# Performance work log

Hardware: AMD Instinct MI355X
Metric: run time of the kernel (lower is better)

The kernel has to match this reference:

```python
import jax, jax.numpy as jnp
import numpy as np

B, L, N, FA, FB, D, OUT, R, T = 128, 128, 6, 39, 10, 200, 1, 3, 2
MB = 256  # num bonds per molecule
NEG = -9e8


def setup_inputs():
    key = jax.random.key(0)
    ks = iter(jax.random.split(key, 64))
    def rn(shape, sc=0.05):
        return jax.random.normal(next(ks), shape, dtype=jnp.float32) * sc
    inp = {}
    inp['atom_list'] = jax.random.normal(next(ks), (B, L, FA), dtype=jnp.float32)
    inp['bond_list'] = jax.random.normal(next(ks), (B, MB, FB), dtype=jnp.float32)
    inp['atom_degree_list'] = jax.random.randint(next(ks), (B, L, N), 0, L, dtype=jnp.int32)
    inp['bond_degree_list'] = jax.random.randint(next(ks), (B, L, N), 0, MB, dtype=jnp.int32)
    inp['atom_mask'] = jnp.ones((B, L), dtype=jnp.float32)
    # parameters (torch Linear: y = x @ W + b with W stored here as [in, out])
    inp['W_atom'] = rn((FA, D)); inp['b_atom'] = rn((D,))
    inp['W_nei'] = rn((FA + FB, D)); inp['b_nei'] = rn((D,))
    inp['W_align'] = rn((R, 2 * D, 1)); inp['b_align'] = rn((R, 1))
    inp['W_attend'] = rn((R, D, D)); inp['b_attend'] = rn((R, D))
    # GRUCell weights, torch layout [3D, D], gate order r,z,n
    inp['Wih'] = rn((R, 3 * D, D)); inp['Whh'] = rn((R, 3 * D, D))
    inp['bih'] = rn((R, 3 * D)); inp['bhh'] = rn((R, 3 * D))
    inp['W_mol_align'] = rn((2 * D, 1)); inp['b_mol_align'] = rn((1,))
    inp['W_mol_attend'] = rn((D, D)); inp['b_mol_attend'] = rn((D,))
    inp['mWih'] = rn((3 * D, D)); inp['mWhh'] = rn((3 * D, D))
    inp['mbih'] = rn((3 * D,)); inp['mbhh'] = rn((3 * D,))
    inp['W_metric'] = rn((2 * D, D)); inp['b_metric'] = rn((D,))
    inp['W_out'] = rn((D, OUT)); inp['b_out'] = rn((OUT,))
    return inp


def _gather(feat, idx):
    # feat [B, M, F], idx [B, L, N] -> [B, L, N, F]
    b, l, n = idx.shape
    g = jnp.take_along_axis(feat, idx.reshape(b, l * n)[..., None], axis=1)
    return g.reshape(b, l, n, feat.shape[-1])


def _gru(x, h, Wih, Whh, bih, bhh):
    gi = x @ Wih.T + bih
    gh = h @ Whh.T + bhh
    ir, iz, inn = jnp.split(gi, 3, axis=-1)
    hr, hz, hn = jnp.split(gh, 3, axis=-1)
    r = jax.nn.sigmoid(ir + hr)
    z = jax.nn.sigmoid(iz + hz)
    n = jnp.tanh(inn + r * hn)
    return (1.0 - z) * n + z * h


def reference(atom_list, bond_list, atom_degree_list, bond_degree_list, atom_mask,
              W_atom, b_atom, W_nei, b_nei, W_align, b_align, W_attend, b_attend,
              Wih, Whh, bih, bhh, W_mol_align, b_mol_align, W_mol_attend, b_mol_attend,
              mWih, mWhh, mbih, mbhh, W_metric, b_metric, W_out, b_out):
    lrelu = jax.nn.leaky_relu
    b, l, _ = atom_list.shape
    atom_feature = lrelu(atom_list @ W_atom + b_atom)          # [B,L,D]
    atom_nei = _gather(atom_list, atom_degree_list)            # [B,L,N,FA]
    bond_nei = _gather(bond_list, bond_degree_list)            # [B,L,N,FB]
    nei = lrelu(jnp.concatenate([atom_nei, bond_nei], -1) @ W_nei + b_nei)  # [B,L,N,D]

    pad = (atom_degree_list == l - 1)
    attend_mask = (~pad).astype(jnp.float32)[..., None]        # [B,L,N,1]
    softmax_mask = jnp.where(pad, NEG, 0.0)[..., None]         # [B,L,N,1]

    h = atom_feature
    cur = atom_feature
    for r in range(R):
        if r > 0:
            nei = _gather(cur, atom_degree_list)
        exp = jnp.broadcast_to(cur[:, :, None, :], nei.shape)
        align = lrelu(jnp.concatenate([exp, nei], -1) @ W_align[r] + b_align[r])
        w = jax.nn.softmax(align + softmax_mask, axis=-2) * attend_mask
        trans = nei @ W_attend[r] + b_attend[r]
        ctx = jax.nn.elu(jnp.sum(w * trans, axis=-2))          # [B,L,D]
        h = _gru(ctx.reshape(-1, D), h.reshape(-1, D), Wih[r], Whh[r], bih[r], bhh[r]).reshape(b, l, D)
        cur = jax.nn.relu(h)

    am = atom_mask[..., None]                                   # [B,L,1]
    mol_feature = jnp.sum(cur * am, axis=-2)                    # [B,D]
    act_mol = jax.nn.relu(mol_feature)
    mol_softmax_mask = jnp.where(am == 0.0, NEG, 0.0)           # [B,L,1]
    for _ in range(T):
        exp = jnp.broadcast_to(act_mol[:, None, :], cur.shape)
        score = lrelu(jnp.concatenate([exp, cur], -1) @ W_mol_align + b_mol_align)
        w = jax.nn.softmax(score + mol_softmax_mask, axis=-2) * am
        trans = cur @ W_mol_attend + b_mol_attend
        ctx = jax.nn.elu(jnp.sum(w * trans, axis=-2))           # [B,D]
        mol_feature = _gru(ctx, mol_feature, mWih, mWhh, mbih, mbhh)
        act_mol = jax.nn.relu(mol_feature)

    dd = jnp.float32(R - 2)  # leaked python loop var `d` in the original
    feat = jnp.concatenate([mol_feature, mol_feature + dd], -1)
    return (feat @ W_metric + b_metric) @ W_out + b_out


if __name__ == '__main__':
    out = reference(**setup_inputs())
    print(out.shape)
```

## Files before the change

### kernel.cpp

```cpp
#include <hip/hip_runtime.h>
#include <hip/hip_bf16.h>
#include <math.h>
#include <string.h>

#define B_ 128
#define L_ 128
#define N_ 6
#define FA_ 39
#define FB_ 10
#define D_ 200
#define MB_ 256
#define R_ 3
#define T_ 2
#define NEGV -9e8f
#define BL_ (B_*L_)
#define G3D_ (3*D_)
#define FP32TAG 0x3F800000u
#define KP 416
#define NP 896
#define KC 224
#define NC 256

typedef __hip_bfloat16 bf16;
typedef __attribute__((ext_vector_type(8))) short short8;
typedef __attribute__((ext_vector_type(4))) float f32x4;

__device__ __forceinline__ float b2f(const bf16 x){ return __bfloat162float(x); }
__device__ __forceinline__ unsigned short f2b(float v){ bf16 t = __float2bfloat16(v); return *reinterpret_cast<unsigned short*>(&t); }
__device__ __forceinline__ float bu2f(unsigned short u){ unsigned x = ((unsigned)u)<<16; float f; memcpy(&f,&x,4); return f; }
__device__ __forceinline__ float lreluf(float x){ return x>=0.f ? x : 0.01f*x; }
__device__ __forceinline__ float eluf(float x){ return x>0.f ? x : expm1f(x); }
__device__ __forceinline__ float sigmf(float x){ return 1.f/(1.f+expf(-x)); }

#define NSEG 14
struct CvtArgs { const void* src[NSEG]; int ofs[NSEG+1]; };

#define PREPB_N (R_*NP*KP)
#define PREPW_N (R_*NC*KC)
#define PREPM_N (D_*G3D_)
#define PREPT_N 40000
#define PREPE_N 80000
#define CONV_N 23989
#define XHPAD_N (BL_*16)
#define AROWS (BL_ + B_*MB_)
#define A_N (AROWS*64)
#define BI_N (448*64)

struct PrepArgs {
    CvtArgs cvt;
    const void *Wih, *Whh, *Watt, *mWih, *mWhh, *Wmt, *Wme;
    const void *bond, *Wnei, *atom, *Watom;
    float* conv;
    unsigned short *B2t, *WatT, *mTi, *mTh, *Wmt16, *Wme16, *XH, *A16, *Bi16;
    const unsigned* amtag;
    int ew_total;
};

__device__ __forceinline__ float ldd(const void* p, size_t i, bool f32){
    return f32 ? ((const float*)p)[i] : b2f(((const bf16*)p)[i]);
}

__global__ void __launch_bounds__(256) k_prep(PrepArgs A){
    bool f32 = (*A.amtag == FP32TAG);
    int i = blockIdx.x*256 + (int)threadIdx.x;
    if (i >= A.ew_total) return;
    if (i < CONV_N){
        int s = 0;
        while (i >= A.cvt.ofs[s+1]) s++;
        A.conv[i] = ldd(A.cvt.src[s], i - A.cvt.ofs[s], f32);
        return;
    }
    int i2 = i - CONV_N;
    if (i2 < PREPB_N){
        int kk = i2 % KP;
        int rest = i2 / KP;
        int n = rest % NP;
        int r = rest / NP;
        float v = 0.f;
        if (kk < 200){
            if (n < 600) v = ldd(A.Wih, ((size_t)(r*G3D_ + n))*D_ + kk, f32);
        } else if (kk < 400){
            int j = -1;
            if (n < 400) j = n;
            else if (n >= 600 && n < 800) j = n - 200;
            if (j >= 0) v = ldd(A.Whh, ((size_t)(r*G3D_ + j))*D_ + (kk-200), f32);
        }
        A.B2t[i2] = f2b(v);
        return;
    }
    int i3 = i2 - PREPB_N;
    if (i3 < PREPW_N){
        int kk = i3 % KC;
        int rest = i3 / KC;
        int n = rest % NC;
        int r = rest / NC;
        float v = 0.f;
        if (kk < 200 && n < 200) v = ldd(A.Watt, ((size_t)r*D_ + kk)*D_ + n, f32);
        A.WatT[i3] = f2b(v);
        return;
    }
    int i4 = i3 - PREPW_N;
    if (i4 < PREPM_N){
        int j = i4 % G3D_, k = i4 / G3D_;
        size_t si = (size_t)j*D_ + k;
        A.mTi[i4] = f2b(ldd(A.mWih, si, f32));
        A.mTh[i4] = f2b(ldd(A.mWhh, si, f32));
        return;
    }
    int i5 = i4 - PREPM_N;
    if (i5 < PREPT_N){
        A.Wmt16[i5] = f2b(ldd(A.Wmt, i5, f32));
        return;
    }
    int i6 = i5 - PREPT_N;
    if (i6 < PREPE_N){
        A.Wme16[i6] = f2b(ldd(A.Wme, i6, f32));
        return;
    }
    int i7 = i6 - PREPE_N;
    if (i7 < XHPAD_N){
        int al = i7 >> 4, j = i7 & 15;
        A.XH[(size_t)al*KP + 400 + j] = 0;
        return;
    }
    int i8 = i7 - XHPAD_N;
    if (i8 < A_N){
        int row = i8 >> 6, k = i8 & 63;
        float v = 0.f;
        if (row < BL_){
            if (k < FA_) v = ldd(A.atom, (size_t)row*FA_ + k, f32);
        } else {
            int rb = row - BL_;
            if (k >= FA_ && k < FA_+FB_) v = ldd(A.bond, (size_t)rb*FB_ + (k-FA_), f32);
        }
        A.A16[i8] = f2b(v);
        return;
    }
    int i9 = i8 - A_N;
    if (i9 < BI_N){
        int n = i9 >> 6, k = i9 & 63;
        float v = 0.f;
        if (n < 200){
            if (k < FA_) v = ldd(A.Watom, (size_t)k*D_ + n, f32);
        } else if (n < 400){
            if (k < FA_+FB_) v = ldd(A.Wnei, (size_t)k*D_ + (n-200), f32);
        }
        A.Bi16[i9] = f2b(v);
    }
}

__global__ void __launch_bounds__(256) k_initmm(const unsigned short* __restrict__ A16,
        const unsigned short* __restrict__ Bi16,
        const void* __restrict__ batom, const void* __restrict__ bnei,
        unsigned short* __restrict__ XH, unsigned short* __restrict__ P16,
        unsigned short* __restrict__ Q16, const unsigned* __restrict__ amtag){
    __shared__ unsigned short As[128][40];
    __shared__ unsigned short Bs[64][40];
    bool f32 = (*amtag == FP32TAG);
    int tid = threadIdx.x;
    int mt = (int)blockIdx.x / 7, nt = (int)blockIdx.x % 7;
    int m0 = mt*128, n0 = nt*64;
    if (m0 >= BL_ && n0 + 64 <= 200) return;
    int lane = tid & 63, wv = tid >> 6;
    int quad = lane >> 4, lm = lane & 15;
    f32x4 acc[2][4];
    #pragma unroll
    for (int a=0;a<2;a++)
        #pragma unroll
        for (int b=0;b<4;b++) acc[a][b] = (f32x4){0.f,0.f,0.f,0.f};
    for (int ks = 0; ks < 2; ks++){
        int r0_ = tid >> 2, c0 = (tid & 3) * 8;
        int r1_ = (tid + 256) >> 2, c1 = ((tid + 256) & 3) * 8;
        uint4 a0 = *(const uint4*)&A16[(size_t)(m0 + r0_)*64 + ks*32 + c0];
        uint4 a1 = *(const uint4*)&A16[(size_t)(m0 + r1_)*64 + ks*32 + c1];
        uint4 b0 = *(const uint4*)&Bi16[(size_t)(n0 + (tid >> 2))*64 + ks*32 + (tid & 3)*8];
        __syncthreads();
        *(uint4*)&As[r0_][c0] = a0;
        *(uint4*)&As[r1_][c1] = a1;
        *(uint4*)&Bs[tid >> 2][(tid & 3)*8] = b0;
        __syncthreads();
        short8 av0 = *(const short8*)&As[wv*32 + lm][quad*8];
        short8 av1 = *(const short8*)&As[wv*32 + 16 + lm][quad*8];
        #pragma unroll
        for (int ns=0; ns<4; ns++){
            short8 bv = *(const short8*)&Bs[ns*16 + lm][quad*8];
            acc[0][ns] = __builtin_amdgcn_mfma_f32_16x16x32_bf16(av0, bv, acc[0][ns], 0,0,0);
            acc[1][ns] = __builtin_amdgcn_mfma_f32_16x16x32_bf16(av1, bv, acc[1][ns], 0,0,0);
        }
    }
    #pragma unroll
    for (int ms=0; ms<2; ms++)
      #pragma unroll
      for (int ns=0; ns<4; ns++){
        int n = n0 + ns*16 + lm;
        #pragma unroll
        for (int i=0;i<4;i++){
            int row = m0 + wv*32 + ms*16 + quad*4 + i;
            float v = acc[ms][ns][i];
            if (row < BL_){
                if (n < 200){
                    XH[(size_t)row*KP + 200 + n] = f2b(lreluf(v + ldd(batom, n, f32)));
                } else if (n < 400){
                    P16[(size_t)row*D_ + (n-200)] = f2b(v + ldd(bnei, n-200, f32));
                }
            } else if (n >= 200 && n < 400){
                Q16[(size_t)(row-BL_)*D_ + (n-200)] = f2b(v);
            }
        }
      }
}

__global__ void __launch_bounds__(256) k_attn(
        const unsigned short* __restrict__ cur16, const unsigned short* __restrict__ XH,
        const float* __restrict__ s1, const float* __restrict__ tb,
        const int* __restrict__ adl, const int* __restrict__ bdl,
        const unsigned short* __restrict__ P16, const unsigned short* __restrict__ Q16,
        const float* __restrict__ W_align, const float* __restrict__ b_align, int r,
        unsigned short* __restrict__ wnei, float* __restrict__ wsum){
    int bid = blockIdx.x;
    int mol = bid & (B_-1), chunk = bid >> 7;
    int wv = threadIdx.x >> 6, lane = threadIdx.x & 63;
    int al = mol*L_ + chunk*4 + wv;
    __shared__ float s_nei[4][N_][D_];

    int idxn[N_]; bool pad[N_];
    for (int n=0;n<N_;n++){ idxn[n] = adl[al*N_ + n]; pad[n] = (idxn[n] == L_-1); }

    float s2[N_];
    float s1v;
    if (r == 0){
        for (int j = lane; j < N_*D_; j += 64){
            int n = j / D_, d = j - n*D_;
            int bd = bdl[al*N_ + n];
            float acc = bu2f(P16[((size_t)mol*L_ + idxn[n])*D_ + d])
                      + bu2f(Q16[((size_t)mol*MB_ + bd)*D_ + d]);
            s_nei[wv][n][d] = lreluf(acc);
        }
        const float* Wab = W_align + D_;
        for (int n=0;n<N_;n++){
            float acc = 0.f;
            for (int d=lane; d<D_; d+=64) acc += s_nei[wv][n][d] * Wab[d];
            for (int o=32;o>0;o>>=1) acc += __shfl_xor(acc,o);
            s2[n] = acc;
        }
        float a1 = 0.f;
        for (int d=lane; d<D_; d+=64) a1 += bu2f(XH[(size_t)al*KP + 200 + d]) * W_align[d];
        for (int o=32;o>0;o>>=1) a1 += __shfl_xor(a1,o);
        s1v = a1;
    } else {
        float tmp = 0.f;
        if (lane < N_) tmp = tb[mol*L_ + idxn[lane]];
        for (int n=0;n<N_;n++) s2[n] = __shfl(tmp, n);
        s1v = s1[al];
    }

    float bav = b_align[r];
    float a[N_]; float mx = -1e30f;
    for (int n=0;n<N_;n++){
        float v = lreluf(s1v + s2[n] + bav);
        if (pad[n]) v += NEGV;
        a[n] = v; mx = fmaxf(mx, v);
    }
    float w[N_]; float se = 0.f;
    for (int n=0;n<N_;n++){ float e = expf(a[n]-mx); w[n]=e; se += e; }
    float inv = 1.f/se; float wsv = 0.f;
    for (int n=0;n<N_;n++){ w[n] = pad[n] ? 0.f : w[n]*inv; wsv += w[n]; }

    if (r == 0){
        for (int d=lane; d<D_; d+=64){
            float acc = 0.f;
            #pragma unroll
            for (int n=0;n<N_;n++) acc += w[n] * s_nei[wv][n][d];
            wnei[(size_t)al*KC + d] = f2b(acc);
        }
    } else {
        for (int d=lane; d<D_; d+=64){
            float acc = 0.f;
            #pragma unroll
            for (int n=0;n<N_;n++) acc += w[n] * bu2f(cur16[((size_t)mol*L_ + idxn[n])*KC + d]);
            wnei[(size_t)al*KC + d] = f2b(acc);
        }
    }
    if (lane < 24) wnei[(size_t)al*KC + 200 + lane] = 0;
    if (lane==0) wsum[al] = wsv;
}

__global__ void __launch_bounds__(256) k_ctxmfma(const unsigned short* __restrict__ Wn,
        const float* __restrict__ wsum, const unsigned short* __restrict__ WatT,
        const float* __restrict__ bias, int r, unsigned short* __restrict__ XH){
    __shared__ unsigned short As[128][40];
    __shared__ unsigned short Bs[64][40];
    int tid = threadIdx.x;
    int m0 = ((int)blockIdx.x & 127) * 128;
    int n0 = ((int)blockIdx.x >> 7) * 64;
    const unsigned short* Bt = WatT + (size_t)r*NC*KC;
    int lane = tid & 63, wv = tid >> 6;
    int quad = lane >> 4, lm = lane & 15;
    f32x4 acc[2][4];
    #pragma unroll
    for (int a=0;a<2;a++)
        #pragma unroll
        for (int b=0;b<4;b++) acc[a][b] = (f32x4){0.f,0.f,0.f,0.f};
    for (int ks = 0; ks < 7; ks++){
        int r0_ = tid >> 2, c0 = (tid & 3) * 8;
        int r1_ = (tid + 256) >> 2, c1 = ((tid + 256) & 3) * 8;
        uint4 a0 = *(const uint4*)&Wn[(size_t)(m0 + r0_)*KC + ks*32 + c0];
        uint4 a1 = *(const uint4*)&Wn[(size_t)(m0 + r1_)*KC + ks*32 + c1];
        uint4 b0 = *(const uint4*)&Bt[(size_t)(n0 + (tid >> 2))*KC + ks*32 + (tid & 3)*8];
        __syncthreads();
        *(uint4*)&As[r0_][c0] = a0;
        *(uint4*)&As[r1_][c1] = a1;
        *(uint4*)&Bs[tid >> 2][(tid & 3)*8] = b0;
        __syncthreads();
        short8 av0 = *(const short8*)&As[wv*32 + lm][quad*8];
        short8 av1 = *(const short8*)&As[wv*32 + 16 + lm][quad*8];
        #pragma unroll
        for (int ns=0; ns<4; ns++){
            short8 bv = *(const short8*)&Bs[ns*16 + lm][quad*8];
            acc[0][ns] = __builtin_amdgcn_mfma_f32_16x16x32_bf16(av0, bv, acc[0][ns], 0,0,0);
            acc[1][ns] = __builtin_amdgcn_mfma_f32_16x16x32_bf16(av1, bv, acc[1][ns], 0,0,0);
        }
    }
    #pragma unroll
    for (int ms=0; ms<2; ms++)
      #pragma unroll
      for (int ns=0; ns<4; ns++){
        int n = n0 + ns*16 + lm;
        if (n < 200){
            float bv = bias[r*D_ + n];
            #pragma unroll
            for (int i=0;i<4;i++){
                int row = m0 + wv*32 + ms*16 + quad*4 + i;
                float v = acc[ms][ns][i] + wsum[row]*bv;
                XH[(size_t)row*KP + n] = f2b(eluf(v));
            }
        }
      }
}

__global__ void __launch_bounds__(256) k_gemm(const unsigned short* __restrict__ XH,
        const unsigned short* __restrict__ B2t, unsigned short* __restrict__ C, int r){
    __shared__ unsigned short As[128][40];
    __shared__ unsigned short Bs[128][40];
    int tid = threadIdx.x;
    int m0 = ((int)blockIdx.x & 127) * 128;
    int n0 = ((int)blockIdx.x >> 7) * 128;
    const unsigned short* Bt = B2t + (size_t)r*NP*KP;
    int lane = tid & 63, wv = tid >> 6;
    int quad = lane >> 4, lm = lane & 15;
    f32x4 acc[2][8];
    #pragma unroll
    for (int a=0;a<2;a++)
        #pragma unroll
        for (int b=0;b<8;b++) acc[a][b] = (f32x4){0.f,0.f,0.f,0.f};
    for (int ks = 0; ks < 13; ks++){
        int r0_ = tid >> 2, c0 = (tid & 3) * 8;
        int r1_ = (tid + 256) >> 2, c1 = ((tid + 256) & 3) * 8;
        uint4 a0 = *(const uint4*)&XH[(size_t)(m0 + r0_)*KP + ks*32 + c0];
        uint4 a1 = *(const uint4*)&XH[(size_t)(m0 + r1_)*KP + ks*32 + c1];
        uint4 b0 = *(const uint4*)&Bt[(size_t)(n0 + r0_)*KP + ks*32 + c0];
        uint4 b1 = *(const uint4*)&Bt[(size_t)(n0 + r1_)*KP + ks*32 + c1];
        __syncthreads();
        *(uint4*)&As[r0_][c0] = a0;
        *(uint4*)&As[r1_][c1] = a1;
        *(uint4*)&Bs[r0_][c0] = b0;
        *(uint4*)&Bs[r1_][c1] = b1;
        __syncthreads();
        short8 av0 = *(const short8*)&As[wv*32 + lm][quad*8];
        short8 av1 = *(const short8*)&As[wv*32 + 16 + lm][quad*8];
        #pragma unroll
        for (int ns=0; ns<8; ns++){
            short8 bv = *(const short8*)&Bs[ns*16 + lm][quad*8];
            acc[0][ns] = __builtin_amdgcn_mfma_f32_16x16x32_bf16(av0, bv, acc[0][ns], 0,0,0);
            acc[1][ns] = __builtin_amdgcn_mfma_f32_16x16x32_bf16(av1, bv, acc[1][ns], 0,0,0);
        }
    }
    #pragma unroll
    for (int ms=0; ms<2; ms++)
      #pragma unroll
      for (int ns=0; ns<8; ns++)
        #pragma unroll
        for (int i=0;i<4;i++){
            int row = m0 + wv*32 + ms*16 + quad*4 + i;
            C[(size_t)row*NP + n0 + ns*16 + lm] = f2b(acc[ms][ns][i]);
        }
}

__global__ void __launch_bounds__(256) k_gru2(const unsigned short* __restrict__ C,
        unsigned short* __restrict__ XH, unsigned short* __restrict__ cur16,
        const float* __restrict__ bih, const float* __restrict__ bhh,
        const float* __restrict__ W_align, const float* __restrict__ Wma, int r,
        float* __restrict__ s1, float* __restrict__ tb, float* __restrict__ curdot){
    int wv = threadIdx.x >> 6, lane = threadIdx.x & 63;
    int al = blockIdx.x*4 + wv;
    size_t base = (size_t)al*NP;
    const float* bi = bih + r*G3D_;
    const float* bh = bhh + r*G3D_;
    const float* Wa = W_align + (r+1)*2*D_;
    bool last = (r == R_-1);
    float a1 = 0.f, a2 = 0.f;
    for (int j = lane; j < D_; j += 64){
        float rsum = bu2f(C[base + j]);
        float zsum = bu2f(C[base + 200 + j]);
        float gin  = bu2f(C[base + 400 + j]);
        float ghn  = bu2f(C[base + 600 + j]);
        float rr = sigmf(rsum + bi[j] + bh[j]);
        float zz = sigmf(zsum + bi[D_+j] + bh[D_+j]);
        float nn = tanhf(gin + bi[2*D_+j] + rr*(ghn + bh[2*D_+j]));
        size_t hx = (size_t)al*KP + 200 + j;
        float hv = bu2f(XH[hx]);
        float hn = (1.f-zz)*nn + zz*hv;
        XH[hx] = f2b(hn);
        float cv = fmaxf(hn, 0.f);
        cur16[(size_t)al*KC + j] = f2b(cv);
        if (last){
            a1 += cv * Wma[D_+j];
        } else {
            a1 += cv * Wa[j];
            a2 += cv * Wa[D_+j];
        }
    }
    if (lane < 24) cur16[(size_t)al*KC + 200 + lane] = 0;
    for (int o=32;o>0;o>>=1){ a1 += __shfl_xor(a1,o); a2 += __shfl_xor(a2,o); }
    if (lane==0){
        if (last) curdot[al] = a1;
        else { s1[al] = a1; tb[al] = a2; }
    }
}

__device__ __forceinline__ float brSum(float v, float* s_red){
    for (int o=32;o>0;o>>=1) v += __shfl_xor(v,o);
    int lane = threadIdx.x & 63, wid = threadIdx.x >> 6;
    __syncthreads();
    if (lane==0) s_red[wid] = v;
    __syncthreads();
    float r = 0.f;
    int nw = blockDim.x >> 6;
    for (int i=0;i<nw;i++) r += s_red[i];
    return r;
}

__device__ __forceinline__ float brMax(float v, float* s_red){
    for (int o=32;o>0;o>>=1) v = fmaxf(v, __shfl_xor(v,o));
    int lane = threadIdx.x & 63, wid = threadIdx.x >> 6;
    __syncthreads();
    if (lane==0) s_red[wid] = v;
    __syncthreads();
    float r = s_red[0];
    int nw = blockDim.x >> 6;
    for (int i=1;i<nw;i++) r = fmaxf(r, s_red[i]);
    return r;
}

__global__ void __launch_bounds__(512) k_mol(const unsigned short* __restrict__ cur16,
    const float* __restrict__ curdot, const float* __restrict__ atom_mask,
    const float* __restrict__ Wma, const float* __restrict__ bma,
    const unsigned short* __restrict__ Wmt16, const float* __restrict__ bmt,
    const unsigned short* __restrict__ mTi, const unsigned short* __restrict__ mTh,
    const float* __restrict__ mbih, const float* __restrict__ mbhh,
    const unsigned short* __restrict__ Wme16, const float* __restrict__ bme,
    const float* __restrict__ Wout, const float* __restrict__ bout,
    void* __restrict__ out, const unsigned* __restrict__ amtag){
    int b = blockIdx.x, tid = threadIdx.x;
    int dq = tid & 255, cq = tid >> 8;
    __shared__ unsigned short s_cur[L_*KC];
    __shared__ float s_am[L_], s_neg[L_], s_cd[L_], s_w[L_];
    __shared__ float s_mf[D_], s_act[D_], s_wc[D_], s_ctx[D_];
    __shared__ float s_gi[G3D_], s_gh[G3D_];
    __shared__ float s_part[2][256];
    __shared__ float s_red[8];
    const uint4* src = (const uint4*)(cur16 + (size_t)b*L_*KC);
    for (int i = tid; i < L_*KC/8; i += 512) ((uint4*)s_cur)[i] = src[i];
    if (tid < L_){
        float am = atom_mask[b*L_ + tid];
        s_am[tid] = am;
        s_neg[tid] = (am == 0.f) ? NEGV : 0.f;
        s_cd[tid] = curdot[b*L_ + tid];
    }
    __syncthreads();
    {
        float a0 = 0.f, a1 = 0.f;
        if (dq < D_)
            for (int l=cq*64; l<cq*64+64; l+=2){
                a0 += bu2f(s_cur[l*KC + dq]) * s_am[l];
                a1 += bu2f(s_cur[(l+1)*KC + dq]) * s_am[l+1];
            }
        s_part[cq][dq] = a0 + a1;
        __syncthreads();
        if (tid < D_){
            float v = s_part[0][tid] + s_part[1][tid];
            s_mf[tid] = v; s_act[tid] = fmaxf(v, 0.f);
        }
        __syncthreads();
    }
    float bma0 = bma[0];
    for (int t=0;t<T_;t++){
        float p = (tid < D_) ? s_act[tid] * Wma[tid] : 0.f;
        float s1v = brSum(p, s_red);
        float sc = (tid < L_) ? (lreluf(s1v + s_cd[tid] + bma0) + s_neg[tid]) : -1e30f;
        float mx = brMax(sc, s_red);
        float e = (tid < L_) ? expf(sc - mx) : 0.f;
        float se = brSum(e, s_red);
        float wv_ = (tid < L_) ? e/se*s_am[tid] : 0.f;
        if (tid < L_) s_w[tid] = wv_;
        float wsm = brSum(wv_, s_red);
        __syncthreads();
        {
            float a0 = 0.f, a1 = 0.f;
            if (dq < D_)
                for (int l=cq*64; l<cq*64+64; l+=2){
                    a0 += s_w[l] * bu2f(s_cur[l*KC + dq]);
                    a1 += s_w[l+1] * bu2f(s_cur[(l+1)*KC + dq]);
                }
            s_part[cq][dq] = a0 + a1;
            __syncthreads();
            if (tid < D_) s_wc[tid] = s_part[0][tid] + s_part[1][tid];
            __syncthreads();
        }
        {
            float a0 = 0.f, a1 = 0.f;
            if (dq < D_)
                for (int k=cq*100; k<cq*100+100; k+=2){
                    a0 += s_wc[k] * bu2f(Wmt16[(size_t)k*D_ + dq]);
                    a1 += s_wc[k+1] * bu2f(Wmt16[(size_t)(k+1)*D_ + dq]);
                }
            s_part[cq][dq] = a0 + a1;
            __syncthreads();
            if (tid < D_)
                s_ctx[tid] = eluf(s_part[0][tid] + s_part[1][tid] + wsm * bmt[tid]);
            __syncthreads();
        }
        for (int j=tid; j<G3D_; j+=512){
            float ai0=0.f, ai1=0.f, ai2=0.f, ai3=0.f;
            float ah0=0.f, ah1=0.f, ah2=0.f, ah3=0.f;
            for (int k=0;k<D_;k+=4){
                ai0 += s_ctx[k]   * bu2f(mTi[(size_t)k*G3D_ + j]);
                ai1 += s_ctx[k+1] * bu2f(mTi[(size_t)(k+1)*G3D_ + j]);
                ai2 += s_ctx[k+2] * bu2f(mTi[(size_t)(k+2)*G3D_ + j]);
                ai3 += s_ctx[k+3] * bu2f(mTi[(size_t)(k+3)*G3D_ + j]);
                ah0 += s_mf[k]    * bu2f(mTh[(size_t)k*G3D_ + j]);
                ah1 += s_mf[k+1]  * bu2f(mTh[(size_t)(k+1)*G3D_ + j]);
                ah2 += s_mf[k+2]  * bu2f(mTh[(size_t)(k+2)*G3D_ + j]);
                ah3 += s_mf[k+3]  * bu2f(mTh[(size_t)(k+3)*G3D_ + j]);
            }
            s_gi[j] = (ai0+ai1)+(ai2+ai3); s_gh[j] = (ah0+ah1)+(ah2+ah3);
        }
        __syncthreads();
        if (tid < D_){
            int d = tid;
            float rr = sigmf(s_gi[d] + mbih[d] + s_gh[d] + mbhh[d]);
            float zz = sigmf(s_gi[D_+d] + mbih[D_+d] + s_gh[D_+d] + mbhh[D_+d]);
            float nn = tanhf(s_gi[2*D_+d] + mbih[2*D_+d] + rr*(s_gh[2*D_+d] + mbhh[2*D_+d]));
            float nm = (1.f-zz)*nn + zz*s_mf[d];
            s_mf[d] = nm; s_act[d] = fmaxf(nm, 0.f);
        }
        __syncthreads();
    }
    const float dd = (float)(R_ - 2);
    {
        float a0 = 0.f, a1 = 0.f;
        if (dq < D_)
            for (int k=cq*100; k<cq*100+100; k+=2){
                float mf0 = s_mf[k], mf1 = s_mf[k+1];
                a0 += mf0 * bu2f(Wme16[(size_t)k*D_ + dq])
                    + (mf0 + dd) * bu2f(Wme16[(size_t)(D_+k)*D_ + dq]);
                a1 += mf1 * bu2f(Wme16[(size_t)(k+1)*D_ + dq])
                    + (mf1 + dd) * bu2f(Wme16[(size_t)(D_+k+1)*D_ + dq]);
            }
        s_part[cq][dq] = a0 + a1;
        __syncthreads();
        float p = 0.f;
        if (tid < D_)
            p = (s_part[0][tid] + s_part[1][tid] + bme[tid]) * Wout[tid];
        float o = brSum(p, s_red);
        if (tid==0){
            o += bout[0];
            if (*amtag == FP32TAG) ((float*)out)[b] = o;
            else ((bf16*)out)[b] = __float2bfloat16(o);
        }
    }
}

extern "C" void kernel_launch(void* const* d_in, const int* in_sizes, int n_in,
                              void* d_out, int out_size, void* d_ws, size_t ws_size,
                              hipStream_t stream) {
    const int* adl = (const int*)d_in[2];
    const int* bdl = (const int*)d_in[3];
    const unsigned* amtag = (const unsigned*)d_in[4];

    static const int srcidx[NSEG] = {4,9,10,12,15,16,17,18,20,23,24,26,27,28};
    static const int segsz[NSEG]  = {16384,1200,3,600,1800,1800,400,1,200,600,600,200,200,1};
    CvtArgs ca;
    int ofs[NSEG+1]; ofs[0] = 0;
    for (int i=0;i<NSEG;i++){ ca.src[i] = d_in[srcidx[i]]; ca.ofs[i] = ofs[i]; ofs[i+1] = ofs[i] + segsz[i]; }
    ca.ofs[NSEG] = ofs[NSEG];

    float* ws   = (float*)d_ws;
    float* conv = ws;
    unsigned short* XH    = (unsigned short*)(conv + 24000);
    unsigned short* B2t   = XH + (size_t)BL_*KP;
    unsigned short* WatT  = B2t + PREPB_N;
    unsigned short* mTi   = WatT + PREPW_N;
    unsigned short* mTh   = mTi + PREPM_N;
    unsigned short* Wmt16 = mTh + PREPM_N;
    unsigned short* Wme16 = Wmt16 + PREPT_N;
    unsigned short* Bi16  = Wme16 + PREPE_N;
    unsigned short* cur16 = Bi16 + BI_N;
    unsigned short* creg  = cur16 + (size_t)BL_*KC;
    unsigned short* C = creg;
    unsigned short* A16  = creg;
    unsigned short* wnei = creg;
    unsigned short* Q16  = creg + (size_t)BL_*KC;
    unsigned short* P16  = Q16 + (size_t)B_*MB_*D_;
    float* s1     = (float*)(creg + (size_t)BL_*NP);
    float* tb     = s1 + BL_;
    float* wsum   = tb + BL_;
    float* curdot = wsum + BL_;

    const float* c_amask = conv + ofs[0];
    const float* c_Walign= conv + ofs[1];
    const float* c_balign= conv + ofs[2];
    const float* c_batt  = conv + ofs[3];
    const float* c_bih   = conv + ofs[4];
    const float* c_bhh   = conv + ofs[5];
    const float* c_Wma   = conv + ofs[6];
    const float* c_bma   = conv + ofs[7];
    const float* c_bmt   = conv + ofs[8];
    const float* c_mbih  = conv + ofs[9];
    const float* c_mbhh  = conv + ofs[10];
    const float* c_bme   = conv + ofs[11];
    const float* c_Wout  = conv + ofs[12];
    const float* c_bout  = conv + ofs[13];

    PrepArgs A;
    A.cvt = ca;
    A.Wih = d_in[13]; A.Whh = d_in[14]; A.Watt = d_in[11];
    A.mWih = d_in[21]; A.mWhh = d_in[22]; A.Wmt = d_in[19]; A.Wme = d_in[25];
    A.bond = d_in[1]; A.Wnei = d_in[7]; A.atom = d_in[0]; A.Watom = d_in[5];
    A.conv = conv;
    A.B2t = B2t; A.WatT = WatT; A.mTi = mTi; A.mTh = mTh;
    A.Wmt16 = Wmt16; A.Wme16 = Wme16; A.XH = XH; A.A16 = A16; A.Bi16 = Bi16;
    A.amtag = amtag;
    A.ew_total = CONV_N + PREPB_N + PREPW_N + PREPM_N + PREPT_N + PREPE_N
               + XHPAD_N + A_N + BI_N;

    k_prep<<<(A.ew_total + 255)/256, 256, 0, stream>>>(A);
    k_initmm<<<(AROWS/128)*7, 256, 0, stream>>>(A16, Bi16, d_in[6], d_in[8],
                                                XH, P16, Q16, amtag);

    for (int r=0; r<R_; r++){
        k_attn<<<BL_/4, 256, 0, stream>>>(cur16, XH, s1, tb, adl, bdl, P16, Q16,
                                          c_Walign, c_balign, r, wnei, wsum);
        k_ctxmfma<<<(BL_/128)*(NC/64), 256, 0, stream>>>(wnei, wsum, WatT, c_batt, r, XH);
        k_gemm<<<(BL_/128)*(NP/128), 256, 0, stream>>>(XH, B2t, C, r);
        k_gru2<<<BL_/4, 256, 0, stream>>>(C, XH, cur16, c_bih, c_bhh,
                                          c_Walign, c_Wma, r, s1, tb, curdot);
    }

    k_mol<<<B_, 512, 0, stream>>>(cur16, curdot, c_amask, c_Wma, c_bma, Wmt16, c_bmt,
                                  mTi, mTh, c_mbih, c_mbhh, Wme16, c_bme, c_Wout, c_bout,
                                  d_out, amtag);
}
```

Baseline: 454.5 us.

## Fuse GRU gate epilogue into gate GEMM with interleaved weights and ping-pong hidden buffers

```diff
diff --git a/kernel.cpp b/kernel.cpp
--- a/kernel.cpp
+++ b/kernel.cpp
@@ -41,7 +41,9 @@
 #define PREPT_N 40000
 #define PREPE_N 80000
 #define CONV_N 23989
-#define XHPAD_N (BL_*16)
+#define XHPAD2_N (2*BL_*16)
+#define CURPAD_N (BL_*24)
+#define ZB_N (3*BL_)
 #define AROWS (BL_ + B_*MB_)
 #define A_N (AROWS*64)
 #define BI_N (448*64)
@@ -51,7 +53,8 @@
     const void *Wih, *Whh, *Watt, *mWih, *mWhh, *Wmt, *Wme;
     const void *bond, *Wnei, *atom, *Watom;
     float* conv;
-    unsigned short *B2t, *WatT, *mTi, *mTh, *Wmt16, *Wme16, *XH, *A16, *Bi16;
+    unsigned short *B2t, *WatT, *mTi, *mTh, *Wmt16, *Wme16, *XHa, *XHb, *A16, *Bi16, *cur16;
+    float* zbase;
     const unsigned* amtag;
     int ew_total;
 };
@@ -76,14 +79,20 @@
         int rest = i2 / KP;
         int n = rest % NP;
         int r = rest / NP;
+        int j = n >> 2, c = n & 3;
         float v = 0.f;
-        if (kk < 200){
-            if (n < 600) v = ldd(A.Wih, ((size_t)(r*G3D_ + n))*D_ + kk, f32);
-        } else if (kk < 400){
-            int j = -1;
-            if (n < 400) j = n;
-            else if (n >= 600 && n < 800) j = n - 200;
-            if (j >= 0) v = ldd(A.Whh, ((size_t)(r*G3D_ + j))*D_ + (kk-200), f32);
+        if (j < 200){
+            if (c == 0){
+                if (kk < 200) v = ldd(A.Wih, ((size_t)(r*G3D_ + j))*D_ + kk, f32);
+                else if (kk < 400) v = ldd(A.Whh, ((size_t)(r*G3D_ + j))*D_ + (kk-200), f32);
+            } else if (c == 1){
+                if (kk < 200) v = ldd(A.Wih, ((size_t)(r*G3D_ + 200 + j))*D_ + kk, f32);
+                else if (kk < 400) v = ldd(A.Whh, ((size_t)(r*G3D_ + 200 + j))*D_ + (kk-200), f32);
+            } else if (c == 2){
+                if (kk < 200) v = ldd(A.Wih, ((size_t)(r*G3D_ + 400 + j))*D_ + kk, f32);
+            } else {
+                if (kk >= 200 && kk < 400) v = ldd(A.Whh, ((size_t)(r*G3D_ + 400 + j))*D_ + (kk-200), f32);
+            }
         }
         A.B2t[i2] = f2b(v);
         return;
@@ -108,24 +117,29 @@
         return;
     }
     int i5 = i4 - PREPM_N;
-    if (i5 < PREPT_N){
-        A.Wmt16[i5] = f2b(ldd(A.Wmt, i5, f32));
+    if (i5 < PREPT_N){ A.Wmt16[i5] = f2b(ldd(A.Wmt, i5, f32)); return; }
+    int i6 = i5 - PREPT_N;
+    if (i6 < PREPE_N){ A.Wme16[i6] = f2b(ldd(A.Wme, i6, f32)); return; }
+    int i7 = i6 - PREPE_N;
+    if (i7 < XHPAD2_N){
+        int buf = i7 >> 18;
+        int loc = i7 & (BL_*16 - 1);
+        int al = loc >> 4, p = loc & 15;
+        unsigned short* X = buf ? A.XHb : A.XHa;
+        X[(size_t)al*KP + 400 + p] = 0;
         return;
     }
-    int i6 = i5 - PREPT_N;
-    if (i6 < PREPE_N){
-        A.Wme16[i6] = f2b(ldd(A.Wme, i6, f32));
+    int i8 = i7 - XHPAD2_N;
+    if (i8 < CURPAD_N){
+        int al = i8 / 24, p = i8 - al*24;
+        A.cur16[(size_t)al*KC + 200 + p] = 0;
         return;
     }
-    int i7 = i6 - PREPE_N;
-    if (i7 < XHPAD_N){
-        int al = i7 >> 4, j = i7 & 15;
-        A.XH[(size_t)al*KP + 400 + j] = 0;
-        return;
-    }
-    int i8 = i7 - XHPAD_N;
-    if (i8 < A_N){
-        int row = i8 >> 6, k = i8 & 63;
+    int i9 = i8 - CURPAD_N;
+    if (i9 < ZB_N){ A.zbase[i9] = 0.f; return; }
+    int i10 = i9 - ZB_N;
+    if (i10 < A_N){
+        int row = i10 >> 6, k = i10 & 63;
         float v = 0.f;
         if (row < BL_){
             if (k < FA_) v = ldd(A.atom, (size_t)row*FA_ + k, f32);
@@ -133,19 +147,19 @@
             int rb = row - BL_;
             if (k >= FA_ && k < FA_+FB_) v = ldd(A.bond, (size_t)rb*FB_ + (k-FA_), f32);
         }
-        A.A16[i8] = f2b(v);
+        A.A16[i10] = f2b(v);
         return;
     }
-    int i9 = i8 - A_N;
-    if (i9 < BI_N){
-        int n = i9 >> 6, k = i9 & 63;
+    int i11 = i10 - A_N;
+    if (i11 < BI_N){
+        int n = i11 >> 6, k = i11 & 63;
         float v = 0.f;
         if (n < 200){
             if (k < FA_) v = ldd(A.Watom, (size_t)k*D_ + n, f32);
         } else if (n < 400){
             if (k < FA_+FB_) v = ldd(A.Wnei, (size_t)k*D_ + (n-200), f32);
         }
-        A.Bi16[i9] = f2b(v);
+        A.Bi16[i11] = f2b(v);
     }
 }
 
@@ -287,12 +301,16 @@
 
 __global__ void __launch_bounds__(256) k_ctxmfma(const unsigned short* __restrict__ Wn,
         const float* __restrict__ wsum, const unsigned short* __restrict__ WatT,
-        const float* __restrict__ bias, int r, unsigned short* __restrict__ XH){
+        const float* __restrict__ bias, int r, unsigned short* __restrict__ XH,
+        float* __restrict__ s1z, float* __restrict__ tbz){
     __shared__ unsigned short As[128][40];
     __shared__ unsigned short Bs[64][40];
     int tid = threadIdx.x;
     int m0 = ((int)blockIdx.x & 127) * 128;
     int n0 = ((int)blockIdx.x >> 7) * 64;
+    if (n0 == 0){
+        for (int idx = tid; idx < 128; idx += 256){ s1z[m0+idx] = 0.f; tbz[m0+idx] = 0.f; }
+    }
     const unsigned short* Bt = WatT + (size_t)r*NC*KC;
     int lane = tid & 63, wv = tid >> 6;
     int quad = lane >> 4, lm = lane & 15;
@@ -338,16 +356,29 @@
       }
 }
 
-__global__ void __launch_bounds__(256) k_gemm(const unsigned short* __restrict__ XH,
-        const unsigned short* __restrict__ B2t, unsigned short* __restrict__ C, int r){
+__global__ void __launch_bounds__(256) k_gg(const unsigned short* __restrict__ XHr,
+        const unsigned short* __restrict__ B2t, unsigned short* __restrict__ XHn,
+        unsigned short* __restrict__ cur16,
+        const float* __restrict__ bih, const float* __restrict__ bhh,
+        const float* __restrict__ W_align, const float* __restrict__ Wma, int r,
+        float* __restrict__ s1, float* __restrict__ tb, float* __restrict__ curdot){
     __shared__ unsigned short As[128][40];
     __shared__ unsigned short Bs[128][40];
+    __shared__ unsigned short Cs[128][130];
+    __shared__ unsigned short hs[128][32];
     int tid = threadIdx.x;
     int m0 = ((int)blockIdx.x & 127) * 128;
-    int n0 = ((int)blockIdx.x >> 7) * 128;
+    int nt = (int)blockIdx.x >> 7;
+    int n0 = nt * 128;
+    int jbase = nt * 32;
     const unsigned short* Bt = B2t + (size_t)r*NP*KP;
     int lane = tid & 63, wv = tid >> 6;
     int quad = lane >> 4, lm = lane & 15;
+    for (int idx = tid; idx < 128*4; idx += 256){
+        int row = idx >> 2, ch = idx & 3;
+        if (200 + jbase + ch*8 + 8 <= KP)
+            *(uint4*)&hs[row][ch*8] = *(const uint4*)&XHr[(size_t)(m0+row)*KP + 200 + jbase + ch*8];
+    }
     f32x4 acc[2][8];
     #pragma unroll
     for (int a=0;a<2;a++)
@@ -356,8 +387,8 @@
     for (int ks = 0; ks < 13; ks++){
         int r0_ = tid >> 2, c0 = (tid & 3) * 8;
         int r1_ = (tid + 256) >> 2, c1 = ((tid + 256) & 3) * 8;
-        uint4 a0 = *(const uint4*)&XH[(size_t)(m0 + r0_)*KP + ks*32 + c0];
-        uint4 a1 = *(const uint4*)&XH[(size_t)(m0 + r1_)*KP + ks*32 + c1];
+        uint4 a0 = *(const uint4*)&XHr[(size_t)(m0 + r0_)*KP + ks*32 + c0];
+        uint4 a1 = *(const uint4*)&XHr[(size_t)(m0 + r1_)*KP + ks*32 + c1];
         uint4 b0 = *(const uint4*)&Bt[(size_t)(n0 + r0_)*KP + ks*32 + c0];
         uint4 b1 = *(const uint4*)&Bt[(size_t)(n0 + r1_)*KP + ks*32 + c1];
         __syncthreads();
@@ -380,51 +411,48 @@
       #pragma unroll
       for (int ns=0; ns<8; ns++)
         #pragma unroll
-        for (int i=0;i<4;i++){
-            int row = m0 + wv*32 + ms*16 + quad*4 + i;
-            C[(size_t)row*NP + n0 + ns*16 + lm] = f2b(acc[ms][ns][i]);
-        }
-}
-
-__global__ void __launch_bounds__(256) k_gru2(const unsigned short* __restrict__ C,
-        unsigned short* __restrict__ XH, unsigned short* __restrict__ cur16,
-        const float* __restrict__ bih, const float* __restrict__ bhh,
-        const float* __restrict__ W_align, const float* __restrict__ Wma, int r,
-        float* __restrict__ s1, float* __restrict__ tb, float* __restrict__ curdot){
-    int wv = threadIdx.x >> 6, lane = threadIdx.x & 63;
-    int al = blockIdx.x*4 + wv;
-    size_t base = (size_t)al*NP;
+        for (int i=0;i<4;i++)
+            Cs[wv*32 + ms*16 + quad*4 + i][ns*16 + lm] = f2b(acc[ms][ns][i]);
+    __syncthreads();
+    int jl = tid & 31;
+    int rowb = tid >> 5;
+    int j = jbase + jl;
+    bool jv = (j < 200);
+    bool last = (r == R_-1);
     const float* bi = bih + r*G3D_;
     const float* bh = bhh + r*G3D_;
-    const float* Wa = W_align + (r+1)*2*D_;
-    bool last = (r == R_-1);
-    float a1 = 0.f, a2 = 0.f;
-    for (int j = lane; j < D_; j += 64){
-        float rsum = bu2f(C[base + j]);
-        float zsum = bu2f(C[base + 200 + j]);
-        float gin  = bu2f(C[base + 400 + j]);
-        float ghn  = bu2f(C[base + 600 + j]);
-        float rr = sigmf(rsum + bi[j] + bh[j]);
-        float zz = sigmf(zsum + bi[D_+j] + bh[D_+j]);
-        float nn = tanhf(gin + bi[2*D_+j] + rr*(ghn + bh[2*D_+j]));
-        size_t hx = (size_t)al*KP + 200 + j;
-        float hv = bu2f(XH[hx]);
-        float hn = (1.f-zz)*nn + zz*hv;
-        XH[hx] = f2b(hn);
-        float cv = fmaxf(hn, 0.f);
-        cur16[(size_t)al*KC + j] = f2b(cv);
-        if (last){
-            a1 += cv * Wma[D_+j];
-        } else {
-            a1 += cv * Wa[j];
-            a2 += cv * Wa[D_+j];
-        }
-    }
-    if (lane < 24) cur16[(size_t)al*KC + 200 + lane] = 0;
-    for (int o=32;o>0;o>>=1){ a1 += __shfl_xor(a1,o); a2 += __shfl_xor(a2,o); }
-    if (lane==0){
-        if (last) curdot[al] = a1;
-        else { s1[al] = a1; tb[al] = a2; }
+    float bir=0,biz=0,bin=0,bhr=0,bhz=0,bhn=0,wj=0,wj2=0;
+    if (jv){
+        bir = bi[j]; biz = bi[D_+j]; bin = bi[2*D_+j];
+        bhr = bh[j]; bhz = bh[D_+j]; bhn = bh[2*D_+j];
+        if (!last){ const float* Wa = W_align + (r+1)*2*D_; wj = Wa[j]; wj2 = Wa[D_+j]; }
+        else wj2 = Wma[D_+j];
+    }
+    for (int it=0; it<16; it++){
+        int row = rowb + 8*it;
+        int rowG = m0 + row;
+        float s1p = 0.f, tbp = 0.f;
+        if (jv){
+            float rsum = bu2f(Cs[row][jl*4+0]);
+            float zsum = bu2f(Cs[row][jl*4+1]);
+            float gin  = bu2f(Cs[row][jl*4+2]);
+            float ghn  = bu2f(Cs[row][jl*4+3]);
+            float rr = sigmf(rsum + bir + bhr);
+            float zz = sigmf(zsum + biz + bhz);
+            float nn = tanhf(gin + bin + rr*(ghn + bhn));
+            float hold = bu2f(hs[row][jl]);
+            float hn = (1.f-zz)*nn + zz*hold;
+            XHn[(size_t)rowG*KP + 200 + j] = f2b(hn);
+            float cv = fmaxf(hn, 0.f);
+            cur16[(size_t)rowG*KC + j] = f2b(cv);
+            if (!last){ s1p = cv*wj; tbp = cv*wj2; }
+            else s1p = cv*wj2;
+        }
+        for (int o=16;o>0;o>>=1){ s1p += __shfl_xor(s1p,o); tbp += __shfl_xor(tbp,o); }
+        if (jl == 0){
+            if (!last){ atomicAdd(&s1[rowG], s1p); atomicAdd(&tb[rowG], tbp); }
+            else atomicAdd(&curdot[rowG], s1p);
+        }
     }
 }
 
@@ -597,8 +625,9 @@
 
     float* ws   = (float*)d_ws;
     float* conv = ws;
-    unsigned short* XH    = (unsigned short*)(conv + 24000);
-    unsigned short* B2t   = XH + (size_t)BL_*KP;
+    unsigned short* XHa   = (unsigned short*)(conv + 24000);
+    unsigned short* XHb   = XHa + (size_t)BL_*KP;
+    unsigned short* B2t   = XHb + (size_t)BL_*KP;
     unsigned short* WatT  = B2t + PREPB_N;
     unsigned short* mTi   = WatT + PREPW_N;
     unsigned short* mTh   = mTi + PREPM_N;
@@ -607,15 +636,14 @@
     unsigned short* Bi16  = Wme16 + PREPE_N;
     unsigned short* cur16 = Bi16 + BI_N;
     unsigned short* creg  = cur16 + (size_t)BL_*KC;
-    unsigned short* C = creg;
     unsigned short* A16  = creg;
     unsigned short* wnei = creg;
     unsigned short* Q16  = creg + (size_t)BL_*KC;
     unsigned short* P16  = Q16 + (size_t)B_*MB_*D_;
-    float* s1     = (float*)(creg + (size_t)BL_*NP);
+    float* s1     = (float*)(P16 + (size_t)BL_*D_);
     float* tb     = s1 + BL_;
-    float* wsum   = tb + BL_;
-    float* curdot = wsum + BL_;
+    float* curdot = tb + BL_;
+    float* wsum   = curdot + BL_;
 
     const float* c_amask = conv + ofs[0];
     const float* c_Walign= conv + ofs[1];
@@ -639,22 +667,27 @@
     A.bond = d_in[1]; A.Wnei = d_in[7]; A.atom = d_in[0]; A.Watom = d_in[5];
     A.conv = conv;
     A.B2t = B2t; A.WatT = WatT; A.mTi = mTi; A.mTh = mTh;
-    A.Wmt16 = Wmt16; A.Wme16 = Wme16; A.XH = XH; A.A16 = A16; A.Bi16 = Bi16;
+    A.Wmt16 = Wmt16; A.Wme16 = Wme16; A.XHa = XHa; A.XHb = XHb;
+    A.A16 = A16; A.Bi16 = Bi16; A.cur16 = cur16;
+    A.zbase = s1;
     A.amtag = amtag;
     A.ew_total = CONV_N + PREPB_N + PREPW_N + PREPM_N + PREPT_N + PREPE_N
-               + XHPAD_N + A_N + BI_N;
+               + XHPAD2_N + CURPAD_N + ZB_N + A_N + BI_N;
 
     k_prep<<<(A.ew_total + 255)/256, 256, 0, stream>>>(A);
     k_initmm<<<(AROWS/128)*7, 256, 0, stream>>>(A16, Bi16, d_in[6], d_in[8],
-                                                XH, P16, Q16, amtag);
+                                                XHa, P16, Q16, amtag);
 
     for (int r=0; r<R_; r++){
-        k_attn<<<BL_/4, 256, 0, stream>>>(cur16, XH, s1, tb, adl, bdl, P16, Q16,
+        unsigned short* XH_r = (r & 1) ? XHb : XHa;
+        unsigned short* XH_n = (r & 1) ? XHa : XHb;
+        k_attn<<<BL_/4, 256, 0, stream>>>(cur16, XH_r, s1, tb, adl, bdl, P16, Q16,
                                           c_Walign, c_balign, r, wnei, wsum);
-        k_ctxmfma<<<(BL_/128)*(NC/64), 256, 0, stream>>>(wnei, wsum, WatT, c_batt, r, XH);
-        k_gemm<<<(BL_/128)*(NP/128), 256, 0, stream>>>(XH, B2t, C, r);
-        k_gru2<<<BL_/4, 256, 0, stream>>>(C, XH, cur16, c_bih, c_bhh,
-                                          c_Walign, c_Wma, r, s1, tb, curdot);
+        k_ctxmfma<<<(BL_/128)*(NC/64), 256, 0, stream>>>(wnei, wsum, WatT, c_batt, r,
+                                                         XH_r, s1, tb);
+        k_gg<<<(BL_/128)*(NP/128), 256, 0, stream>>>(XH_r, B2t, XH_n, cur16,
+                                                     c_bih, c_bhh, c_Walign, c_Wma, r,
+                                                     s1, tb, curdot);
     }
 
     k_mol<<<B_, 512, 0, stream>>>(cur16, curdot, c_amask, c_Wma, c_bma, Wmt16, c_bmt,
```

After: 456.0 us. No clear change (+0.3%).
